# Performance work log

Hardware: AMD Instinct MI355X
Metric: run time of the kernel (lower is better)

The kernel has to match this reference:

```python
import jax, jax.numpy as jnp
import numpy as np

K = 3      # kernel size
PAD = 1    # kernel_size // 2


def _deform_conv(x, offset, w_def):
    """mmcv DeformConv (deform_groups=1, stride=1, dilation=1, no bias).
    x: [B,C,H,W], offset: [B,2*K*K,H,W] ordered (dy,dx) per kernel tap, w_def: [O,C,K,K].
    Bilinear sampling with zero padding outside the feature map.
    """
    B, C, H, W = x.shape
    kk = K * K
    off = offset.reshape(B, kk, 2, H, W)
    # kernel-tap grid (row-major: ky, kx)
    ar = jnp.arange(K)
    gy, gx = jnp.meshgrid(ar, ar, indexing='ij')
    gy = gy.reshape(kk)
    gx = gx.reshape(kk)
    hh = jnp.arange(H, dtype=x.dtype)
    ww = jnp.arange(W, dtype=x.dtype)
    # sampling positions: p0 - pad + kernel tap + learned offset  -> [B,kk,H,W]
    ys = hh[None, None, :, None] - PAD + gy[None, :, None, None] + off[:, :, 0]
    xs = ww[None, None, None, :] - PAD + gx[None, :, None, None] + off[:, :, 1]

    y0 = jnp.floor(ys)
    x0 = jnp.floor(xs)
    ly = ys - y0
    lx = xs - x0

    xf = x.reshape(B, C, H * W)

    def gather(yi, xi):
        valid = (yi >= 0) & (yi <= H - 1) & (xi >= 0) & (xi <= W - 1)
        yc = jnp.clip(yi, 0, H - 1).astype(jnp.int32)
        xc = jnp.clip(xi, 0, W - 1).astype(jnp.int32)
        idx = (yc * W + xc).reshape(B, 1, kk * H * W)
        g = jnp.take_along_axis(xf, idx, axis=2).reshape(B, C, kk, H, W)
        return g * valid.reshape(B, 1, kk, H, W).astype(x.dtype)

    # bilinear interpolation, per-corner zero masking == zero padding
    v = (gather(y0, x0) * ((1 - ly) * (1 - lx))[:, None]
         + gather(y0, x0 + 1) * ((1 - ly) * lx)[:, None]
         + gather(y0 + 1, x0) * (ly * (1 - lx))[:, None]
         + gather(y0 + 1, x0 + 1) * (ly * lx)[:, None])  # [B,C,kk,H,W]

    O = w_def.shape[0]
    return jnp.einsum('bckhw,ock->bohw', v, w_def.reshape(O, C, kk))


def setup_inputs() -> dict:
    key = jax.random.key(0)
    k1, k2, k3, k4 = jax.random.split(key, 4)
    B, C_in, C_off, C_out, H, W = 4, 128, 64, 128, 128, 128
    x = jax.random.normal(k1, (B, C_in, H, W), dtype=jnp.float32)
    off = jax.random.normal(k2, (B, C_off, H, W), dtype=jnp.float32)
    # NOTE: the torch module zero-inits the offset conv; we use small random
    # weights so the deformable gather path is actually exercised.
    w_off = 0.1 * jax.random.normal(k3, (2 * K * K, C_off), dtype=jnp.float32)
    b_off = jnp.zeros((2 * K * K,), dtype=jnp.float32)
    w_def = jax.random.normal(k4, (C_out, C_in, K, K), dtype=jnp.float32) / np.sqrt(C_in * K * K)
    return {"x": x, "off": off, "w_off": w_off, "b_off": b_off, "w_def": w_def}


def reference(x, off, w_off, b_off, w_def):
    # 1x1 offset conv
    offset = jnp.einsum('oc,bchw->bohw', w_off, off) + b_off[None, :, None, None]
    # deformable conv + ReLU
    return jax.nn.relu(_deform_conv(x, offset, w_def))
```

## Files before the change

### kernel.cpp

```cpp
#include <hip/hip_runtime.h>
#include <stdint.h>

typedef __attribute__((ext_vector_type(8))) short short8;
typedef __attribute__((ext_vector_type(4))) float f32x4;

constexpr int Hc = 128, Wc = 128, HWc = Hc * Wc;
constexpr int Cin = 128, Cout = 128;
constexpr int OffC = 18, OffIn = 64;

__device__ __forceinline__ float bf2f(unsigned short u) {
    return __builtin_bit_cast(float, (unsigned)u << 16);
}
__device__ __forceinline__ unsigned short f2bf(float f) {
    unsigned u = __builtin_bit_cast(unsigned, f);
    return (unsigned short)((u + 0x7FFFu + ((u >> 16) & 1u)) >> 16);
}

__global__ void k_offconv(const float* __restrict__ off, const float* __restrict__ w_off,
                          const float* __restrict__ b_off, float* __restrict__ offset) {
    __shared__ float wsm[OffC * OffIn];
    __shared__ float bsm[OffC];
    int tid = threadIdx.x;
    for (int i = tid; i < OffC * OffIn; i += 256) wsm[i] = w_off[i];
    if (tid < OffC) bsm[tid] = b_off[tid];
    __syncthreads();
    int g = blockIdx.x * 256 + tid;
    int b = g >> 14, hw = g & (HWc - 1);
    const float* offb = off + b * OffIn * HWc + hw;
    float acc[OffC];
#pragma unroll
    for (int o = 0; o < OffC; ++o) acc[o] = bsm[o];
    for (int c = 0; c < OffIn; ++c) {
        float v = offb[c << 14];
#pragma unroll
        for (int o = 0; o < OffC; ++o) acc[o] += wsm[o * OffIn + c] * v;
    }
    float* outb = offset + b * OffC * HWc + hw;
#pragma unroll
    for (int o = 0; o < OffC; ++o) outb[o << 14] = acc[o];
}

__global__ void k_xpose(const float* __restrict__ x, unsigned short* __restrict__ xt) {
    __shared__ float tile[128][65];
    int blk = blockIdx.x;
    int b = blk >> 8;
    int hw0 = (blk & 255) << 6;
    const float* xb = x + b * Cin * HWc;
    int tid = threadIdx.x;
#pragma unroll
    for (int k = 0; k < 32; ++k) {
        int e = tid + k * 256;
        int c = e >> 6, p = e & 63;
        tile[c][p] = xb[(c << 14) + hw0 + p];
    }
    __syncthreads();
    unsigned short* xtb = xt + ((b << 14) + hw0) * Cin;
#pragma unroll
    for (int k = 0; k < 16; ++k) {
        int e = (tid + k * 256) * 2;
        int p = e >> 7, c = e & 127;
        unsigned lo = f2bf(tile[c][p]);
        unsigned hi = f2bf(tile[c + 1][p]);
        *(unsigned*)(xtb + e) = lo | (hi << 16);
    }
}

__global__ void k_wprep(const float* __restrict__ wd, unsigned short* __restrict__ wt) {
    int i = blockIdx.x * 256 + threadIdx.x;
    int kk = i >> 14, o = (i >> 7) & 127, c = i & 127;
    wt[i] = f2bf(wd[((o << 7) + c) * 9 + kk]);
}

__global__ __launch_bounds__(256)
void k_deform(const unsigned short* __restrict__ xt, const float* __restrict__ offset,
              const unsigned short* __restrict__ wt, float* __restrict__ out) {
    int tid = threadIdx.x;
    int lane = tid & 63, wave = tid >> 6;
    int bid = blockIdx.x;
    int swz = (bid & 7) * 64 + (bid >> 3);
    int b = swz >> 7;
    int hw0 = (swz & 127) << 7;
    int p0 = hw0 + (wave << 5) + (lane & 15);
    int p1 = p0 + 16;
    int cg = lane >> 4;

    const unsigned short* xb = xt + ((size_t)b << 21);
    const float* offp = offset + (size_t)b * (OffC * HWc);

    int h0 = p0 >> 7, w0 = p0 & 127;
    int h1 = p1 >> 7, w1 = p1 & 127;

    f32x4 acc[8][2];
#pragma unroll
    for (int i = 0; i < 8; ++i)
#pragma unroll
        for (int j = 0; j < 2; ++j)
            acc[i][j] = (f32x4){0.f, 0.f, 0.f, 0.f};

    auto cparm = [&](int tap, float dy, float dx, int h, int w, float* cw, int* cb) {
        float ys = (float)(h - 1 + tap / 3) + dy;
        float xs = (float)(w - 1 + tap % 3) + dx;
        float y0f = floorf(ys), x0f = floorf(xs);
        float ly = ys - y0f, lx = xs - x0f;
        int y0 = (int)y0f, x0 = (int)x0f;
#pragma unroll
        for (int cr = 0; cr < 4; ++cr) {
            int yi = y0 + (cr >> 1), xi = x0 + (cr & 1);
            bool valid = (yi >= 0) && (yi < Hc) && (xi >= 0) && (xi < Wc);
            float wy = (cr >> 1) ? ly : 1.0f - ly;
            float wx = (cr & 1) ? lx : 1.0f - lx;
            int yc = yi < 0 ? 0 : (yi > Hc - 1 ? Hc - 1 : yi);
            int xc = xi < 0 ? 0 : (xi > Wc - 1 ? Wc - 1 : xi);
            cw[cr] = valid ? wy * wx : 0.0f;
            cb[cr] = ((yc << 7) + xc) << 7;
        }
    };

    auto blend = [&](const short8* r, const float* cw) -> short8 {
        short8 pk;
#pragma unroll
        for (int j = 0; j < 8; ++j) {
            float v = cw[0] * bf2f((unsigned short)r[0][j])
                    + cw[1] * bf2f((unsigned short)r[1][j])
                    + cw[2] * bf2f((unsigned short)r[2][j])
                    + cw[3] * bf2f((unsigned short)r[3][j]);
            pk[j] = (short)f2bf(v);
        }
        return pk;
    };

    float cw0[4], cw1[4]; int cb0[4], cb1[4];
    float dy0 = offp[p0], dx0 = offp[(1 << 14) + p0];
    float dy1 = offp[p1], dx1 = offp[(1 << 14) + p1];

    for (int t = 0; t < 9; ++t) {
        cparm(t, dy0, dx0, h0, w0, cw0, cb0);
        cparm(t, dy1, dx1, h1, w1, cw1, cb1);
        if (t < 8) {
            dy0 = offp[((2 * t + 2) << 14) + p0]; dx0 = offp[((2 * t + 3) << 14) + p0];
            dy1 = offp[((2 * t + 2) << 14) + p1]; dx1 = offp[((2 * t + 3) << 14) + p1];
        }
        const unsigned short* wtap = wt + (t << 14);
#pragma unroll
        for (int ks = 0; ks < 4; ++ks) {
            int kc = (ks << 5) + (cg << 3);
            short8 r0[4], r1[4];
#pragma unroll
            for (int cr = 0; cr < 4; ++cr) {
                r0[cr] = *(const short8*)(xb + cb0[cr] + kc);
                r1[cr] = *(const short8*)(xb + cb1[cr] + kc);
            }
            short8 A[8];
#pragma unroll
            for (int ot = 0; ot < 8; ++ot)
                A[ot] = *(const short8*)(wtap + ((ot << 4) + (lane & 15)) * 128 + kc);
            short8 bf0 = blend(r0, cw0);
            short8 bf1 = blend(r1, cw1);
#pragma unroll
            for (int ot = 0; ot < 8; ++ot) {
                acc[ot][0] = __builtin_amdgcn_mfma_f32_16x16x32_bf16(A[ot], bf0, acc[ot][0], 0, 0, 0);
                acc[ot][1] = __builtin_amdgcn_mfma_f32_16x16x32_bf16(A[ot], bf1, acc[ot][1], 0, 0, 0);
            }
        }
    }

#pragma unroll
    for (int ot = 0; ot < 8; ++ot)
#pragma unroll
        for (int pt = 0; pt < 2; ++pt)
#pragma unroll
            for (int j = 0; j < 4; ++j) {
                int o = (ot << 4) + ((lane >> 4) << 2) + j;
                int px = hw0 + (wave << 5) + (pt << 4) + (lane & 15);
                float v = acc[ot][pt][j];
                out[(((size_t)(b << 7) + o) << 14) + px] = v > 0.f ? v : 0.f;
            }
}

extern "C" void kernel_launch(void* const* d_in, const int* in_sizes, int n_in,
                              void* d_out, int out_size, void* d_ws, size_t ws_size,
                              hipStream_t stream) {
    const float* x     = (const float*)d_in[0];
    const float* off   = (const float*)d_in[1];
    const float* w_off = (const float*)d_in[2];
    const float* b_off = (const float*)d_in[3];
    const float* w_def = (const float*)d_in[4];
    float* out = (float*)d_out;

    char* ws = (char*)d_ws;
    float* offset      = (float*)ws;
    unsigned short* xt = (unsigned short*)(ws + 4718592);
    unsigned short* wt = (unsigned short*)(ws + 4718592 + 16777216);

    hipLaunchKernelGGL(k_offconv, dim3(256),  dim3(256), 0, stream, off, w_off, b_off, offset);
    hipLaunchKernelGGL(k_xpose,   dim3(1024), dim3(256), 0, stream, x, xt);
    hipLaunchKernelGGL(k_wprep,   dim3(576),  dim3(256), 0, stream, w_def, wt);
    hipLaunchKernelGGL(k_deform,  dim3(512),  dim3(256), 0, stream, xt, offset, wt, out);
}
```

Measured before the change: 240.6 us.

## Halve per-wave pixel tile in deform kernel to raise occupancy and grid size

Each wave now computes one 16-pixel tile instead of two. The grid doubles to 1024 blocks and __launch_bounds__(256,4) requests higher occupancy. The bilinear blend now packs pairs with the packed bf16x2 conversion intrinsic. The aim is to hide the latency of the gather loads through more resident waves and more blocks across CUs. In exchange, each weight A fragment loaded from global memory is reused for half as many MFMAs, which doubles weight load traffic per output.

```diff
diff --git a/kernel.cpp b/kernel.cpp
--- a/kernel.cpp
+++ b/kernel.cpp
@@ -1,4 +1,5 @@
 #include <hip/hip_runtime.h>
+#include <hip/hip_bf16.h>
 #include <stdint.h>
 
 typedef __attribute__((ext_vector_type(8))) short short8;
@@ -71,35 +72,30 @@
     wt[i] = f2bf(wd[((o << 7) + c) * 9 + kk]);
 }
 
-__global__ __launch_bounds__(256)
+__global__ __launch_bounds__(256, 4)
 void k_deform(const unsigned short* __restrict__ xt, const float* __restrict__ offset,
               const unsigned short* __restrict__ wt, float* __restrict__ out) {
     int tid = threadIdx.x;
     int lane = tid & 63, wave = tid >> 6;
     int bid = blockIdx.x;
-    int swz = (bid & 7) * 64 + (bid >> 3);
-    int b = swz >> 7;
-    int hw0 = (swz & 127) << 7;
-    int p0 = hw0 + (wave << 5) + (lane & 15);
-    int p1 = p0 + 16;
+    int swz = (bid & 7) * 128 + (bid >> 3);
+    int b = swz >> 8;
+    int hw0 = (swz & 255) << 6;
+    int p0 = hw0 + (wave << 4) + (lane & 15);
     int cg = lane >> 4;
 
     const unsigned short* xb = xt + ((size_t)b << 21);
     const float* offp = offset + (size_t)b * (OffC * HWc);
 
     int h0 = p0 >> 7, w0 = p0 & 127;
-    int h1 = p1 >> 7, w1 = p1 & 127;
 
-    f32x4 acc[8][2];
+    f32x4 acc[8];
 #pragma unroll
-    for (int i = 0; i < 8; ++i)
-#pragma unroll
-        for (int j = 0; j < 2; ++j)
-            acc[i][j] = (f32x4){0.f, 0.f, 0.f, 0.f};
+    for (int i = 0; i < 8; ++i) acc[i] = (f32x4){0.f, 0.f, 0.f, 0.f};
 
-    auto cparm = [&](int tap, float dy, float dx, int h, int w, float* cw, int* cb) {
-        float ys = (float)(h - 1 + tap / 3) + dy;
-        float xs = (float)(w - 1 + tap % 3) + dx;
+    auto cparm = [&](int tap, float dy, float dx, float* cw, int* cb) {
+        float ys = (float)(h0 - 1 + tap / 3) + dy;
+        float xs = (float)(w0 - 1 + tap % 3) + dx;
         float y0f = floorf(ys), x0f = floorf(xs);
         float ly = ys - y0f, lx = xs - x0f;
         int y0 = (int)y0f, x0 = (int)x0f;
@@ -117,64 +113,61 @@
     };
 
     auto blend = [&](const short8* r, const float* cw) -> short8 {
-        short8 pk;
+        union { unsigned u[4]; short8 s; } pk;
 #pragma unroll
-        for (int j = 0; j < 8; ++j) {
-            float v = cw[0] * bf2f((unsigned short)r[0][j])
-                    + cw[1] * bf2f((unsigned short)r[1][j])
-                    + cw[2] * bf2f((unsigned short)r[2][j])
-                    + cw[3] * bf2f((unsigned short)r[3][j]);
-            pk[j] = (short)f2bf(v);
+        for (int j = 0; j < 4; ++j) {
+            float va = cw[0] * bf2f((unsigned short)r[0][2 * j])
+                     + cw[1] * bf2f((unsigned short)r[1][2 * j])
+                     + cw[2] * bf2f((unsigned short)r[2][2 * j])
+                     + cw[3] * bf2f((unsigned short)r[3][2 * j]);
+            float vb = cw[0] * bf2f((unsigned short)r[0][2 * j + 1])
+                     + cw[1] * bf2f((unsigned short)r[1][2 * j + 1])
+                     + cw[2] * bf2f((unsigned short)r[2][2 * j + 1])
+                     + cw[3] * bf2f((unsigned short)r[3][2 * j + 1]);
+            __hip_bfloat162 h2 = __float22bfloat162_rn(make_float2(va, vb));
+            unsigned r32;
+            __builtin_memcpy(&r32, &h2, 4);
+            pk.u[j] = r32;
         }
-        return pk;
+        return pk.s;
     };
 
-    float cw0[4], cw1[4]; int cb0[4], cb1[4];
+    float cw0[4]; int cb0[4];
     float dy0 = offp[p0], dx0 = offp[(1 << 14) + p0];
-    float dy1 = offp[p1], dx1 = offp[(1 << 14) + p1];
 
     for (int t = 0; t < 9; ++t) {
-        cparm(t, dy0, dx0, h0, w0, cw0, cb0);
-        cparm(t, dy1, dx1, h1, w1, cw1, cb1);
+        cparm(t, dy0, dx0, cw0, cb0);
         if (t < 8) {
-            dy0 = offp[((2 * t + 2) << 14) + p0]; dx0 = offp[((2 * t + 3) << 14) + p0];
-            dy1 = offp[((2 * t + 2) << 14) + p1]; dx1 = offp[((2 * t + 3) << 14) + p1];
+            dy0 = offp[((2 * t + 2) << 14) + p0];
+            dx0 = offp[((2 * t + 3) << 14) + p0];
         }
         const unsigned short* wtap = wt + (t << 14);
 #pragma unroll
         for (int ks = 0; ks < 4; ++ks) {
             int kc = (ks << 5) + (cg << 3);
-            short8 r0[4], r1[4];
+            short8 r0[4];
 #pragma unroll
-            for (int cr = 0; cr < 4; ++cr) {
+            for (int cr = 0; cr < 4; ++cr)
                 r0[cr] = *(const short8*)(xb + cb0[cr] + kc);
-                r1[cr] = *(const short8*)(xb + cb1[cr] + kc);
-            }
             short8 A[8];
 #pragma unroll
             for (int ot = 0; ot < 8; ++ot)
                 A[ot] = *(const short8*)(wtap + ((ot << 4) + (lane & 15)) * 128 + kc);
             short8 bf0 = blend(r0, cw0);
-            short8 bf1 = blend(r1, cw1);
 #pragma unroll
-            for (int ot = 0; ot < 8; ++ot) {
-                acc[ot][0] = __builtin_amdgcn_mfma_f32_16x16x32_bf16(A[ot], bf0, acc[ot][0], 0, 0, 0);
-                acc[ot][1] = __builtin_amdgcn_mfma_f32_16x16x32_bf16(A[ot], bf1, acc[ot][1], 0, 0, 0);
-            }
+            for (int ot = 0; ot < 8; ++ot)
+                acc[ot] = __builtin_amdgcn_mfma_f32_16x16x32_bf16(A[ot], bf0, acc[ot], 0, 0, 0);
         }
     }
 
 #pragma unroll
     for (int ot = 0; ot < 8; ++ot)
 #pragma unroll
-        for (int pt = 0; pt < 2; ++pt)
-#pragma unroll
-            for (int j = 0; j < 4; ++j) {
-                int o = (ot << 4) + ((lane >> 4) << 2) + j;
-                int px = hw0 + (wave << 5) + (pt << 4) + (lane & 15);
-                float v = acc[ot][pt][j];
-                out[(((size_t)(b << 7) + o) << 14) + px] = v > 0.f ? v : 0.f;
-            }
+        for (int j = 0; j < 4; ++j) {
+            int o = (ot << 4) + ((lane >> 4) << 2) + j;
+            float v = acc[ot][j];
+            out[(((size_t)(b << 7) + o) << 14) + p0] = v > 0.f ? v : 0.f;
+        }
 }
 
 extern "C" void kernel_launch(void* const* d_in, const int* in_sizes, int n_in,
@@ -195,5 +188,5 @@
     hipLaunchKernelGGL(k_offconv, dim3(256),  dim3(256), 0, stream, off, w_off, b_off, offset);
     hipLaunchKernelGGL(k_xpose,   dim3(1024), dim3(256), 0, stream, x, xt);
     hipLaunchKernelGGL(k_wprep,   dim3(576),  dim3(256), 0, stream, w_def, wt);
-    hipLaunchKernelGGL(k_deform,  dim3(512),  dim3(256), 0, stream, xt, offset, wt, out);
+    hipLaunchKernelGGL(k_deform,  dim3(1024), dim3(256), 0, stream, xt, offset, wt, out);
 }
```

Result: slower. 302.8 us (+25.8%).
